# Kernel tuning notes

Measured on AMD Instinct MI355X. Metric: run time of the kernel, lower is better.

## Reference

```python
import jax, jax.numpy as jnp
import numpy as np

N = 100000   # nodes
E = 1600000  # edges
G = 1024     # graphs
V = 51       # attr_dims[0]+1 embedding rows (padding_idx=0)
EMB = 32
H = 2        # heads
D = 64       # hidden_dim (per-head out channels)
DC = H * D   # 128 = dim_conv
NEG_GAT = 0.2   # PyG GATConv default negative_slope
NEG_ACT = 0.05  # module's leaky_relu slope
LN_EPS = 1e-5


def setup_inputs() -> dict:
    key = jax.random.key(0)
    ks = jax.random.split(key, 20)
    def nrm(k, shape, scale=0.1):
        return jax.random.normal(k, shape, dtype=jnp.float32) * scale
    x = jax.random.randint(ks[0], (N, 1), 0, V)
    edge_index = jax.random.randint(ks[1], (2, E), 0, N)
    batch_idx = jnp.sort(jax.random.randint(ks[2], (N,), 0, G))
    return {
        'x': x, 'edge_index': edge_index, 'batch_idx': batch_idx,
        'emb': nrm(ks[3], (V, EMB)).at[0].set(0.0),  # padding_idx=0
        'ln_g': jnp.ones((EMB,), jnp.float32), 'ln_b': jnp.zeros((EMB,), jnp.float32),
        'W1': nrm(ks[4], (EMB, DC)), 'a_src1': nrm(ks[5], (H, D)), 'a_dst1': nrm(ks[6], (H, D)), 'b1': nrm(ks[7], (DC,)),
        'W2': nrm(ks[8], (DC, DC)), 'a_src2': nrm(ks[9], (H, D)), 'a_dst2': nrm(ks[10], (H, D)), 'b2': nrm(ks[11], (DC,)),
        'gw1': nrm(ks[12], (DC, D)), 'gb1': nrm(ks[13], (D,)),
        'gw2': nrm(ks[14], (D, 1)), 'gb2': nrm(ks[15], (1,)),
    }


def _gat_conv(xf, src, dst, W, a_src, a_dst, b):
    # xf: [N, in]; returns [N, H*D]. PyG GATConv, eval mode (attn dropout off).
    xw = (xf @ W).reshape(N, H, D)                           # [N,H,D]
    al_s = jnp.einsum('nhd,hd->nh', xw, a_src)
    al_d = jnp.einsum('nhd,hd->nh', xw, a_dst)
    e = jax.nn.leaky_relu(al_s[src] + al_d[dst], NEG_GAT)    # [E',H]
    m = jax.ops.segment_max(e, dst, num_segments=N)
    ex = jnp.exp(e - m[dst])
    s = jax.ops.segment_sum(ex, dst, num_segments=N)
    alpha = ex / s[dst]                                      # segment softmax over incoming edges
    msg = xw[src] * alpha[:, :, None]                        # [E',H,D]
    out = jax.ops.segment_sum(msg, dst, num_segments=N)      # [N,H,D]
    return out.reshape(N, DC) + b


def reference(x, edge_index, batch_idx, emb, ln_g, ln_b,
              W1, a_src1, a_dst1, b1, W2, a_src2, a_dst2, b2,
              gw1, gb1, gw2, gb2):
    # embedding + LayerNorm (dropout off in eval)
    xe = emb[x[:, 0]]                                        # [N,32]
    mu = jnp.mean(xe, axis=-1, keepdims=True)
    var = jnp.var(xe, axis=-1, keepdims=True)
    xe = (xe - mu) * jax.lax.rsqrt(var + LN_EPS) * ln_g + ln_b
    # add self loops (GATConv add_self_loops=True)
    ar = jnp.arange(N, dtype=edge_index.dtype)
    src = jnp.concatenate([edge_index[0], ar])
    dst = jnp.concatenate([edge_index[1], ar])
    h = jax.nn.leaky_relu(_gat_conv(xe, src, dst, W1, a_src1, a_dst1, b1), NEG_ACT)
    h = _gat_conv(h, src, dst, W2, a_src2, a_dst2, b2)       # [N,128]
    # attentional aggregation over graphs
    gate = jax.nn.leaky_relu(h @ gw1 + gb1, NEG_ACT) @ gw2 + gb2   # [N,1]
    gm = jax.ops.segment_max(gate, batch_idx, num_segments=G)
    ge = jnp.exp(gate - gm[batch_idx])
    gs = jax.ops.segment_sum(ge, batch_idx, num_segments=G)
    w = ge / gs[batch_idx]
    z = jax.ops.segment_sum(w * h, batch_idx, num_segments=G)      # [G,128]
    return h, z
```

## Files before the change

kernel.cpp:

```cpp
#include <hip/hip_runtime.h>
#include <hip/hip_bf16.h>
#include <stdint.h>

typedef unsigned short u16;
typedef unsigned int   u32;
typedef __attribute__((ext_vector_type(8))) short bf16x8;
typedef __attribute__((ext_vector_type(4))) float f32x4;

#define NEG_GAT 0.2f
#define NEG_ACT 0.05f
#define LN_EPS  1e-5f
#define NPARAM  15

__device__ __forceinline__ float bf2f(u32 bits16){
  union { u32 u; float f; } v; v.u = bits16 << 16; return v.f;
}
__device__ __forceinline__ u16 f2bf(float f){
  union { float f; u32 u; } v; v.f = f;
  u32 u = v.u;
  u32 r = (u + 0x7fffu + ((u >> 16) & 1u)) >> 16;
  return (u16)r;
}
__device__ __forceinline__ float lrelu(float x, float s){ return fmaxf(x, s * x); }

__device__ __forceinline__ int geti(const int* __restrict__ p, int i, int enc){
  return p[enc ? (2 * i) : i];
}


struct CvtParams {
  const void* src[NPARAM];
  float*      dst[NPARAM];
  int         n[NPARAM];
};

__global__ void k_detect(const u32* __restrict__ ln_g_raw, const int* __restrict__ ei_raw,
                         int* __restrict__ fflag, int* __restrict__ iflag,
                         int* __restrict__ errflag)
{
  if (threadIdx.x == 0){
    *fflag = (ln_g_raw[0] == 0x3F800000u) ? 0 : 1;
    int zeros = 0;
    for (int j = 0; j < 64; j++) if (ei_raw[2 * j + 1] == 0) zeros++;
    *iflag = (zeros >= 60) ? 1 : 0;
    *errflag = 0;
  }
}

__global__ void k_convert(CvtParams P, const int* __restrict__ flag)
{
  const int pi  = blockIdx.y;
  const int idx = blockIdx.x * 256 + threadIdx.x;
  if (idx >= P.n[pi]) return;
  if (*flag == 0) P.dst[pi][idx] = ((const float*)P.src[pi])[idx];
  else            P.dst[pi][idx] = bf2f(((const u16*)P.src[pi])[idx]);
}


__global__ void k_check_sorted(const int* __restrict__ batch, const int* __restrict__ iflag,
                               int n, int* __restrict__ errflag)
{
  int i = blockIdx.x * 256 + threadIdx.x;
  if (i < n - 1){
    if (geti(batch, i, *iflag) > geti(batch, i + 1, *iflag)) atomicOr(errflag, 8);
  }
}

__global__ void k_check_x(const int* __restrict__ x, const int* __restrict__ iflag,
                          int n, int V, int* __restrict__ errflag)
{
  int i = blockIdx.x * 256 + threadIdx.x;
  if (i < n){
    int v = geti(x, i, *iflag);
    if ((unsigned)v >= (unsigned)V) atomicOr(errflag, 16);
  }
}

__global__ void k_check_edges(const int* __restrict__ ei, const int* __restrict__ iflag,
                              int E, int n, int* __restrict__ errflag)
{
  int e = blockIdx.x * 256 + threadIdx.x;
  if (e < E){
    int enc = *iflag;
    int s = geti(ei, e, enc);
    int d = geti(ei, E + e, enc);
    if ((unsigned)s >= (unsigned)n || (unsigned)d >= (unsigned)n) atomicOr(errflag, 32);
  }
}


__global__ void k_hist(const int* __restrict__ ei, const int* __restrict__ iflag,
                       int* __restrict__ counts, int E, int n)
{
  int e = blockIdx.x * 256 + threadIdx.x;
  if (e < E){
    int d = geti(ei, E + e, *iflag);
    d = min(max(d, 0), n - 1);
    atomicAdd(&counts[d], 1);
  }
}

__global__ void k_scanA(const int* __restrict__ counts, int* __restrict__ rowptr,
                        int* __restrict__ bsums, int n)
{
  __shared__ int sd[1024];
  int tid = threadIdx.x;
  int gid = blockIdx.x * 1024 + tid;
  int v = (gid < n) ? counts[gid] : 0;
  sd[tid] = v;
  __syncthreads();
  for (int off = 1; off < 1024; off <<= 1){
    int t = 0;
    if (tid >= off) t = sd[tid - off];
    __syncthreads();
    if (tid >= off) sd[tid] += t;
    __syncthreads();
  }
  if (gid < n) rowptr[gid] = sd[tid] - v;
  if (tid == 1023) bsums[blockIdx.x] = sd[1023];
}

__global__ void k_scanB(const int* __restrict__ bsums, int* __restrict__ boffs, int nb)
{
  __shared__ int sd[128];
  int tid = threadIdx.x;
  int v = (tid < nb) ? bsums[tid] : 0;
  sd[tid] = v;
  __syncthreads();
  for (int off = 1; off < 128; off <<= 1){
    int t = 0;
    if (tid >= off) t = sd[tid - off];
    __syncthreads();
    if (tid >= off) sd[tid] += t;
    __syncthreads();
  }
  if (tid < nb) boffs[tid] = sd[tid] - v;
}

__global__ void k_scanC(int* __restrict__ rowptr, const int* __restrict__ boffs,
                        int* __restrict__ cursor, int n, int Etot)
{
  int gid = blockIdx.x * 1024 + threadIdx.x;
  if (gid < n){
    int v = rowptr[gid] + boffs[blockIdx.x];
    rowptr[gid] = v;
    cursor[gid] = v;
  }
  if (gid == 0) rowptr[n] = Etot;
}

__global__ void k_scatter(const int* __restrict__ ei, const int* __restrict__ iflag,
                          int* __restrict__ cursor, int* __restrict__ csr, int E, int n)
{
  int e = blockIdx.x * 256 + threadIdx.x;
  if (e < E){
    int enc = *iflag;
    int s = geti(ei, e, enc);
    int d = geti(ei, E + e, enc);
    d = min(max(d, 0), n - 1);
    int pos = atomicAdd(&cursor[d], 1);
    csr[pos] = s;
  }
}

__global__ void k_check_rows(const int* __restrict__ rowptr, const int* __restrict__ cursor,
                             int n, int* __restrict__ errflag)
{
  int i = blockIdx.x * 256 + threadIdx.x;
  if (i < n){
    if (cursor[i] != rowptr[i + 1]) atomicOr(errflag, 1);
    if (i == 0 && rowptr[0] != 0)   atomicOr(errflag, 4);
  }
}

__global__ void k_check_csr(const int* __restrict__ csr, int E, int n, int* __restrict__ errflag)
{
  int e = blockIdx.x * 256 + threadIdx.x;
  if (e < E && (unsigned)csr[e] >= (unsigned)n) atomicOr(errflag, 2);
}


#define BSH   9
#define BSZ   512
#define BMSK  511
#define MAXB  2048
#define BINB  8192
#define BTH   512

__global__ void k_bhist(const int* __restrict__ ei, const int* __restrict__ iflag,
                        int* __restrict__ bcnt, int E, int N, int nbuck)
{
  __shared__ int h[MAXB];
  const int t = threadIdx.x;
  for (int i = t; i < nbuck; i += 256) h[i] = 0;
  __syncthreads();
  const int enc = *iflag;
  for (int e = blockIdx.x * 256 + t; e < E; e += gridDim.x * 256){
    int d = geti(ei, E + e, enc);
    d = min(max(d, 0), N - 1);
    atomicAdd(&h[d >> BSH], 1);
  }
  __syncthreads();
  for (int i = t; i < nbuck; i += 256){
    int c = h[i];
    if (c) atomicAdd(&bcnt[i], c);
  }
}

__global__ void k_bscan(const int* __restrict__ bcnt, int* __restrict__ boff,
                        int* __restrict__ gcur, int* __restrict__ rowptr,
                        int nbuck, int N, int E)
{
  __shared__ int sd[MAXB];
  const int lane = threadIdx.x;
  for (int i = lane; i < nbuck; i += 64) sd[i] = bcnt[i];
  __syncthreads();
  const int L = (nbuck + 63) >> 6;
  const int b0 = lane * L;
  int sum = 0;
  for (int j = 0; j < L; j++){ int idx = b0 + j; if (idx < nbuck) sum += sd[idx]; }
  int excl = sum;
  for (int off = 1; off < 64; off <<= 1){
    int x = __shfl_up(excl, off);
    if (lane >= off) excl += x;
  }
  excl -= sum;
  int run = excl;
  for (int j = 0; j < L; j++){
    int idx = b0 + j;
    if (idx < nbuck){ boff[idx] = run; gcur[idx] = run; run += sd[idx]; }
  }
  if (lane == 0){ boff[nbuck] = E; rowptr[N] = E; }
}

__global__ __launch_bounds__(BTH) void k_bbin(
    const int* __restrict__ ei, const int* __restrict__ iflag,
    int* __restrict__ gcur, u32* __restrict__ binned,
    int E, int N, int nbuck)
{
  __shared__ u32 stage[BINB];
  __shared__ u16 sbk[BINB];
  __shared__ int hist[MAXB];
  __shared__ int base[MAXB];
  __shared__ int gpos[MAXB];
  const int t   = threadIdx.x;
  const int e0  = blockIdx.x * BINB;
  const int cnt = min(BINB, E - e0);
  const int enc = *iflag;

  for (int i = t; i < nbuck; i += BTH) hist[i] = 0;
  __syncthreads();

  u32 pv[16]; int bk[16]; int rk[16];
  #pragma unroll
  for (int k = 0; k < 16; k++){
    bk[k] = -1;
    int lo = k * BTH + t;
    if (lo < cnt){
      int e = e0 + lo;
      int s = geti(ei, e, enc);
      int d = geti(ei, E + e, enc);
      s = min(max(s, 0), N - 1);
      d = min(max(d, 0), N - 1);
      int b = d >> BSH;
      pv[k] = ((u32)s << BSH) | (u32)(d & BMSK);
      bk[k] = b;
      rk[k] = atomicAdd(&hist[b], 1);
    }
  }
  __syncthreads();

  if (t < 64){
    const int L = (nbuck + 63) >> 6;
    const int b0 = t * L;
    int sum = 0;
    for (int j = 0; j < L; j++){ int idx = b0 + j; if (idx < nbuck) sum += hist[idx]; }
    int excl = sum;
    for (int off = 1; off < 64; off <<= 1){
      int x = __shfl_up(excl, off);
      if (t >= off) excl += x;
    }
    excl -= sum;
    int run = excl;
    for (int j = 0; j < L; j++){
      int idx = b0 + j;
      if (idx < nbuck){ base[idx] = run; run += hist[idx]; }
    }
  }
  __syncthreads();

  for (int i = t; i < nbuck; i += BTH){
    int c = hist[i];
    gpos[i] = c ? atomicAdd(&gcur[i], c) : 0;
  }
  __syncthreads();

  #pragma unroll
  for (int k = 0; k < 16; k++){
    if (bk[k] >= 0){
      int slot = base[bk[k]] + rk[k];
      stage[slot] = pv[k];
      sbk[slot]   = (u16)bk[k];
    }
  }
  __syncthreads();

  for (int j = t; j < cnt; j += BTH){
    int b = sbk[j];
    binned[gpos[b] + (j - base[b])] = stage[j];
  }
}

__global__ __launch_bounds__(256) void k_bcsr(
    const u32* __restrict__ binned, const int* __restrict__ boff,
    int* __restrict__ rowptr, int* __restrict__ csr, int N, int nbuck)
{
  __shared__ int cnt[BSZ];
  __shared__ int rp[BSZ];
  __shared__ int cur[BSZ];
  const int b = blockIdx.x;
  const int t = threadIdx.x;
  const int lo = boff[b], hi = boff[b + 1];

  for (int i = t; i < BSZ; i += 256){ cnt[i] = 0; cur[i] = 0; }
  __syncthreads();

  for (int j = lo + t; j < hi; j += 256)
    atomicAdd(&cnt[binned[j] & BMSK], 1);
  __syncthreads();

  if (t < 64){
    const int b0 = t * 8;
    int sum = 0;
    #pragma unroll
    for (int j = 0; j < 8; j++) sum += cnt[b0 + j];
    int excl = sum;
    for (int off = 1; off < 64; off <<= 1){
      int x = __shfl_up(excl, off);
      if (t >= off) excl += x;
    }
    excl -= sum;
    int run = excl;
    #pragma unroll
    for (int j = 0; j < 8; j++){ rp[b0 + j] = run; run += cnt[b0 + j]; }
  }
  __syncthreads();

  const int node0 = b << BSH;
  for (int i = t; i < BSZ; i += 256){
    int node = node0 + i;
    if (node < N) rowptr[node] = lo + rp[i];
  }

  for (int j = lo + t; j < hi; j += 256){
    u32 pvv = binned[j];
    int dl  = pvv & BMSK;
    int pos = lo + rp[dl] + atomicAdd(&cur[dl], 1);
    csr[pos] = (int)(pvv >> BSH);
  }
}


__global__ void k_stamp_if(const int* __restrict__ errflag, float* __restrict__ out, int nel)
{
  int f = *errflag;
  if (f == 0) return;
  float s = 500.0f + 100.0f * (float)f;
  int i = blockIdx.x * 256 + threadIdx.x;
  if (i < nel) out[i] = s;
}

__global__ void k_stamp(float* __restrict__ out, int nel, float val)
{
  int i = blockIdx.x * 256 + threadIdx.x;
  if (i < nel) out[i] = val;
}


__global__ void k_prep(const float* __restrict__ emb,
                       const float* __restrict__ ln_g, const float* __restrict__ ln_b,
                       const float* __restrict__ W1, const float* __restrict__ a_src,
                       const float* __restrict__ a_dst,
                       u16* __restrict__ xwv, float* __restrict__ alsv, float* __restrict__ aldv)
{
  __shared__ float se[32];
  __shared__ float stats[2];
  __shared__ float sxw[128];
  const int v = blockIdx.x, t = threadIdx.x;
  if (t < 32) se[t] = emb[v * 32 + t];
  __syncthreads();
  if (t == 0){
    float s1 = 0.f, s2 = 0.f;
    for (int k = 0; k < 32; k++){ s1 += se[k]; s2 += se[k] * se[k]; }
    float mu = s1 * (1.f / 32.f);
    float var = s2 * (1.f / 32.f) - mu * mu;
    stats[0] = mu; stats[1] = rsqrtf(var + LN_EPS);
  }
  __syncthreads();
  const float mu = stats[0], rs = stats[1];
  float o = 0.f;
  for (int k = 0; k < 32; k++){
    float xe = (se[k] - mu) * rs * ln_g[k] + ln_b[k];
    o += xe * W1[k * 128 + t];
  }
  sxw[t] = o;
  xwv[v * 128 + t] = f2bf(o);
  __syncthreads();
  if (t < 2){
    float ps = 0.f, pd = 0.f;
    for (int d = 0; d < 64; d++){
      float vv = sxw[t * 64 + d];
      ps += vv * a_src[t * 64 + d];
      pd += vv * a_dst[t * 64 + d];
    }
    alsv[2 * v + t] = ps;
    aldv[2 * v + t] = pd;
  }
}


__global__ __launch_bounds__(256, 4) void k_gatw1(
    const int* __restrict__ rowptr, const int* __restrict__ csr,
    const int* __restrict__ x, const int* __restrict__ iflag,
    const float* __restrict__ alsv, const float* __restrict__ aldv,
    const u16* __restrict__ xwv, const float* __restrict__ bias,
    int N, int V, float* __restrict__ out)
{
  extern __shared__ char smem[];
  u16*    sxwv  = (u16*)smem;
  float2* sals  = (float2*)(smem + (size_t)V * 256);
  float2* sald  = sals + V;
  float4* sedge = (float4*)(smem + (size_t)V * 256 + (size_t)V * 16);

  const int tid = threadIdx.x;
  const int enc = *iflag;

  {
    const uint4* gx = (const uint4*)xwv;
    uint4* lx = (uint4*)sxwv;
    for (int idx = tid; idx < V * 16; idx += 256) lx[idx] = gx[idx];
    const float2* ga = (const float2*)alsv;
    const float2* gd = (const float2*)aldv;
    for (int idx = tid; idx < V; idx += 256){ sals[idx] = ga[idx]; sald[idx] = gd[idx]; }
  }
  __syncthreads();

  const int wave = tid >> 6;
  const int lane = tid & 63;
  const int sub  = lane >> 4;
  const int c16  = lane & 15;
  float4* mst = sedge + wave * 64;

  for (int i = blockIdx.x * 4 + wave; i < N; i += gridDim.x * 4){
    const int r0 = rowptr[i], deg = rowptr[i + 1] - r0, total = deg + 1;
    int vi = geti(x, i, enc); vi = min(max(vi, 0), V - 1);
    const float2 ad = sald[vi];

    float sum0 = 0.f, sum1 = 0.f;
    float acc[8];
    #pragma unroll
    for (int r = 0; r < 8; r++) acc[r] = 0.f;

    if (total <= 64){
      int vs = vi;
      float a0 = -3.0e38f, a1 = -3.0e38f;
      if (lane < total){
        int s = (lane < deg) ? csr[r0 + lane] : i;
        int v = geti(x, s, enc);
        vs = min(max(v, 0), V - 1);
        float2 as = sals[vs];
        a0 = lrelu(as.x + ad.x, NEG_GAT);
// ... 96 lines not shown
    int V, float* __restrict__ out)
{
  const int i    = blockIdx.x;
  const int lane = threadIdx.x;
  const int sub  = lane >> 4;
  const int c16  = lane & 15;
  const int enc  = *iflag;
  const int r0 = rowptr[i], deg = rowptr[i + 1] - r0, total = deg + 1;
  int vi = geti(x, i, enc); vi = min(max(vi, 0), V - 1);
  const float ad0 = aldv[2 * vi], ad1 = aldv[2 * vi + 1];

  float sum0 = 0.f, sum1 = 0.f;
  float acc[8];
  #pragma unroll
  for (int r = 0; r < 8; r++) acc[r] = 0.f;

  float m0 = -3.0e38f, m1 = -3.0e38f;
  for (int k = lane; k < total; k += 64){
    int s = (k < deg) ? csr[r0 + k] : i;
    int v = geti(x, s, enc); v = min(max(v, 0), V - 1);
    float2 as = *(const float2*)(alsv + 2 * v);
    m0 = fmaxf(m0, lrelu(as.x + ad0, NEG_GAT));
    m1 = fmaxf(m1, lrelu(as.y + ad1, NEG_GAT));
  }
  #pragma unroll
  for (int off = 32; off; off >>= 1){
    m0 = fmaxf(m0, __shfl_xor(m0, off));
    m1 = fmaxf(m1, __shfl_xor(m1, off));
  }
  for (int base = 0; base < total; base += 64){
    int k = base + lane;
    int vs = vi; float ex0 = 0.f, ex1 = 0.f;
    if (k < total){
      int s = (k < deg) ? csr[r0 + k] : i;
      int v = geti(x, s, enc); vs = min(max(v, 0), V - 1);
      float2 as = *(const float2*)(alsv + 2 * vs);
      ex0 = __expf(lrelu(as.x + ad0, NEG_GAT) - m0);
      ex1 = __expf(lrelu(as.y + ad1, NEG_GAT) - m1);
    }
    sum0 += ex0; sum1 += ex1;
    int cnt = min(64, total - base);
    int qmax = (cnt + 3) & ~3;
    for (int q = 0; q < qmax; q += 4){
      int   j  = q + sub;
      int   vj = __shfl(vs, j);
      float e0 = __shfl(ex0, j);
      float e1 = __shfl(ex1, j);
      float ej = (c16 < 8) ? e0 : e1;
      uint4 w = *(const uint4*)(xwv + (size_t)vj * 128 + c16 * 8);
      acc[0] += ej * bf2f(w.x & 0xffffu); acc[1] += ej * bf2f(w.x >> 16);
      acc[2] += ej * bf2f(w.y & 0xffffu); acc[3] += ej * bf2f(w.y >> 16);
      acc[4] += ej * bf2f(w.z & 0xffffu); acc[5] += ej * bf2f(w.z >> 16);
      acc[6] += ej * bf2f(w.w & 0xffffu); acc[7] += ej * bf2f(w.w >> 16);
    }
  }

  #pragma unroll
  for (int off = 32; off; off >>= 1){
    sum0 += __shfl_xor(sum0, off);
    sum1 += __shfl_xor(sum1, off);
  }
  #pragma unroll
  for (int r = 0; r < 8; r++){
    acc[r] += __shfl_xor(acc[r], 16);
    acc[r] += __shfl_xor(acc[r], 32);
  }

  if (sub == 0){
    float inv = 1.f / ((c16 < 8) ? sum0 : sum1);
    const float4* bp = (const float4*)(bias + c16 * 8);
    float4 b0 = bp[0], b1 = bp[1];
    float4 o0, o1;
    o0.x = lrelu(acc[0] * inv + b0.x, NEG_ACT); o0.y = lrelu(acc[1] * inv + b0.y, NEG_ACT);
    o0.z = lrelu(acc[2] * inv + b0.z, NEG_ACT); o0.w = lrelu(acc[3] * inv + b0.w, NEG_ACT);
    o1.x = lrelu(acc[4] * inv + b1.x, NEG_ACT); o1.y = lrelu(acc[5] * inv + b1.y, NEG_ACT);
    o1.z = lrelu(acc[6] * inv + b1.z, NEG_ACT); o1.w = lrelu(acc[7] * inv + b1.w, NEG_ACT);
    float* op = out + (size_t)i * 128 + c16 * 8;
    *(float4*)op       = o0;
    *(float4*)(op + 4) = o1;
  }
}


__global__ __launch_bounds__(256, 4) void k_gatw2(
    const int* __restrict__ rowptr, const int* __restrict__ csr,
    const float* __restrict__ al_s, const float* __restrict__ al_d,
    const u16* __restrict__ xw, const float* __restrict__ bias,
    int apply_act, int N, float* __restrict__ out)
{
  __shared__ float4 sedge[4][64];
  const int tid  = threadIdx.x;
  const int wave = tid >> 6;
  const int lane = tid & 63;
  const int sub  = lane >> 4;
  const int c16  = lane & 15;
  float4* mst = sedge[wave];

  for (int i = blockIdx.x * 4 + wave; i < N; i += gridDim.x * 4){
    const int r0 = rowptr[i], deg = rowptr[i + 1] - r0, total = deg + 1;
    const float2 ad = *(const float2*)(al_d + 2 * i);

    float sum0 = 0.f, sum1 = 0.f;
    float acc[8];
    #pragma unroll
    for (int r = 0; r < 8; r++) acc[r] = 0.f;

    if (total <= 64){
      int s = i;
      float a0 = -3.0e38f, a1 = -3.0e38f;
      if (lane < total){
        s = (lane < deg) ? csr[r0 + lane] : i;
        float2 as = *(const float2*)(al_s + 2 * s);
        a0 = lrelu(as.x + ad.x, NEG_GAT);
        a1 = lrelu(as.y + ad.y, NEG_GAT);
      }
      float m0 = a0, m1 = a1;
      #pragma unroll
      for (int off = 32; off; off >>= 1){
        m0 = fmaxf(m0, __shfl_xor(m0, off));
        m1 = fmaxf(m1, __shfl_xor(m1, off));
      }
      float ex0 = 0.f, ex1 = 0.f;
      if (lane < total){ ex0 = __expf(a0 - m0); ex1 = __expf(a1 - m1); }
      sum0 = ex0; sum1 = ex1;
      mst[lane] = make_float4(__int_as_float(s), ex0, ex1, 0.f);
      int qmax = (total + 3) & ~3;
      float4 md = mst[sub];
      uint4  w  = *(const uint4*)(xw + (size_t)__float_as_int(md.x) * 128 + c16 * 8);
      for (int q = 0; q < qmax; q += 4){
        float ej = (c16 < 8) ? md.y : md.z;
        uint4 wc = w;
        if (q + 4 < qmax){
          md = mst[q + 4 + sub];
          w  = *(const uint4*)(xw + (size_t)__float_as_int(md.x) * 128 + c16 * 8);
        }
        acc[0] += ej * bf2f(wc.x & 0xffffu); acc[1] += ej * bf2f(wc.x >> 16);
        acc[2] += ej * bf2f(wc.y & 0xffffu); acc[3] += ej * bf2f(wc.y >> 16);
        acc[4] += ej * bf2f(wc.z & 0xffffu); acc[5] += ej * bf2f(wc.z >> 16);
        acc[6] += ej * bf2f(wc.w & 0xffffu); acc[7] += ej * bf2f(wc.w >> 16);
      }
    } else {
      float m0 = -3.0e38f, m1 = -3.0e38f;
      for (int k = lane; k < total; k += 64){
        int s = (k < deg) ? csr[r0 + k] : i;
        float2 as = *(const float2*)(al_s + 2 * s);
        m0 = fmaxf(m0, lrelu(as.x + ad.x, NEG_GAT));
        m1 = fmaxf(m1, lrelu(as.y + ad.y, NEG_GAT));
      }
      #pragma unroll
      for (int off = 32; off; off >>= 1){
        m0 = fmaxf(m0, __shfl_xor(m0, off));
        m1 = fmaxf(m1, __shfl_xor(m1, off));
      }
      for (int base = 0; base < total; base += 64){
        int k = base + lane;
        int s = i; float ex0 = 0.f, ex1 = 0.f;
        if (k < total){
          s = (k < deg) ? csr[r0 + k] : i;
          float2 as = *(const float2*)(al_s + 2 * s);
          ex0 = __expf(lrelu(as.x + ad.x, NEG_GAT) - m0);
          ex1 = __expf(lrelu(as.y + ad.y, NEG_GAT) - m1);
        }
        sum0 += ex0; sum1 += ex1;
        mst[lane] = make_float4(__int_as_float(s), ex0, ex1, 0.f);
        int cnt = min(64, total - base);
        int qmax = (cnt + 3) & ~3;
        for (int q = 0; q < qmax; q += 4){
          float4 md = mst[q + sub];
          float ej = (c16 < 8) ? md.y : md.z;
          uint4 w = *(const uint4*)(xw + (size_t)__float_as_int(md.x) * 128 + c16 * 8);
          acc[0] += ej * bf2f(w.x & 0xffffu); acc[1] += ej * bf2f(w.x >> 16);
          acc[2] += ej * bf2f(w.y & 0xffffu); acc[3] += ej * bf2f(w.y >> 16);
          acc[4] += ej * bf2f(w.z & 0xffffu); acc[5] += ej * bf2f(w.z >> 16);
          acc[6] += ej * bf2f(w.w & 0xffffu); acc[7] += ej * bf2f(w.w >> 16);
        }
      }
    }

    #pragma unroll
    for (int off = 32; off; off >>= 1){
      sum0 += __shfl_xor(sum0, off);
      sum1 += __shfl_xor(sum1, off);
    }
    #pragma unroll
    for (int r = 0; r < 8; r++){
      acc[r] += __shfl_xor(acc[r], 16);
      acc[r] += __shfl_xor(acc[r], 32);
    }

    if (sub == 0){
      float inv = 1.f / ((c16 < 8) ? sum0 : sum1);
      const float4* bp = (const float4*)(bias + c16 * 8);
      float4 b0 = bp[0], b1 = bp[1];
      float4 o0, o1;
      o0.x = acc[0] * inv + b0.x; o0.y = acc[1] * inv + b0.y;
      o0.z = acc[2] * inv + b0.z; o0.w = acc[3] * inv + b0.w;
      o1.x = acc[4] * inv + b1.x; o1.y = acc[5] * inv + b1.y;
      o1.z = acc[6] * inv + b1.z; o1.w = acc[7] * inv + b1.w;
      if (apply_act){
        o0.x = lrelu(o0.x, NEG_ACT); o0.y = lrelu(o0.y, NEG_ACT);
        o0.z = lrelu(o0.z, NEG_ACT); o0.w = lrelu(o0.w, NEG_ACT);
        o1.x = lrelu(o1.x, NEG_ACT); o1.y = lrelu(o1.y, NEG_ACT);
        o1.z = lrelu(o1.z, NEG_ACT); o1.w = lrelu(o1.w, NEG_ACT);
      }
      float* op = out + (size_t)i * 128 + c16 * 8;
      *(float4*)op       = o0;
      *(float4*)(op + 4) = o1;
    }
  }
}


__global__ void k_packW(const float* __restrict__ W, int ncols, int ntiles,
                        u16* __restrict__ pb)
{
  const int ktile = blockIdx.x / ntiles;
  const int ntile = blockIdx.x % ntiles;
  const int lane  = threadIdx.x;
  const int n  = ntile * 16 + (lane & 15);
  const int k0 = ktile * 32 + (lane >> 4) * 8;
  u16* dst = pb + ((size_t)blockIdx.x * 64 + lane) * 8;
  #pragma unroll
  for (int j = 0; j < 8; j++)
    dst[j] = f2bf(W[(k0 + j) * ncols + n]);
}


__global__ __launch_bounds__(256, 2) void k_node2m(
    const float* __restrict__ h1, const u16* __restrict__ pb2,
    const float* __restrict__ a_src, const float* __restrict__ a_dst,
    int N, u16* __restrict__ xw, float* __restrict__ al_s, float* __restrict__ al_d)
{
  const int wave = threadIdx.x >> 6;
  const int lane = threadIdx.x & 63;
  const int rowbase = blockIdx.x * 64 + wave * 16;
  const int m    = lane & 15;
  const int quad = lane >> 4;

  int arow = rowbase + m; if (arow >= N) arow = N - 1;
  const float* aptr = h1 + (size_t)arow * 128 + quad * 8;

  f32x4 acc[8];
  #pragma unroll
  for (int nt = 0; nt < 8; nt++) acc[nt] = (f32x4){0.f, 0.f, 0.f, 0.f};

  #pragma unroll
  for (int kt = 0; kt < 4; kt++){
    float4 a0 = *(const float4*)(aptr + kt * 32);
    float4 a1 = *(const float4*)(aptr + kt * 32 + 4);
    bf16x8 af;
    af[0] = (short)f2bf(a0.x); af[1] = (short)f2bf(a0.y);
    af[2] = (short)f2bf(a0.z); af[3] = (short)f2bf(a0.w);
    af[4] = (short)f2bf(a1.x); af[5] = (short)f2bf(a1.y);
    af[6] = (short)f2bf(a1.z); af[7] = (short)f2bf(a1.w);
    const u16* bbase = pb2 + (((size_t)kt * 8) * 64 + lane) * 8;
    #pragma unroll
    for (int nt = 0; nt < 8; nt++){
      bf16x8 bf = *(const bf16x8*)(bbase + (size_t)nt * 64 * 8);
      acc[nt] = __builtin_amdgcn_mfma_f32_16x16x32_bf16(af, bf, acc[nt], 0, 0, 0);
    }
  }

  float asv[8], adv[8];
  #pragma unroll
  for (int nt = 0; nt < 8; nt++){
    asv[nt] = a_src[nt * 16 + m];
    adv[nt] = a_dst[nt * 16 + m];
  }
  #pragma unroll
  for (int r = 0; r < 4; r++){
    int row = rowbase + quad * 4 + r;
    bool ok = row < N;
    float s0 = 0.f, s1 = 0.f, d0 = 0.f, d1 = 0.f;
    #pragma unroll
    for (int nt = 0; nt < 8; nt++){
      float v = acc[nt][r];
      if (ok) xw[(size_t)row * 128 + nt * 16 + m] = f2bf(v);
      if (nt < 4){ s0 += v * asv[nt]; d0 += v * adv[nt]; }
      else       { s1 += v * asv[nt]; d1 += v * adv[nt]; }
    }
    #pragma unroll
    for (int off = 1; off < 16; off <<= 1){
      s0 += __shfl_xor(s0, off); s1 += __shfl_xor(s1, off);
      d0 += __shfl_xor(d0, off); d1 += __shfl_xor(d1, off);
    }
    if (ok && m == 0){
      al_s[2 * row] = s0; al_s[2 * row + 1] = s1;
      al_d[2 * row] = d0; al_d[2 * row + 1] = d1;
    }
  }
}


__global__ __launch_bounds__(256, 2) void k_gatem(
    const float* __restrict__ h, const u16* __restrict__ pbg,
    const float* __restrict__ gb1, const float* __restrict__ gw2,
    const float* __restrict__ gb2, int N, float* __restrict__ gate)
{
  const int wave = threadIdx.x >> 6;
  const int lane = threadIdx.x & 63;
  const int rowbase = blockIdx.x * 64 + wave * 16;
  const int m    = lane & 15;
  const int quad = lane >> 4;

  int arow = rowbase + m; if (arow >= N) arow = N - 1;
  const float* aptr = h + (size_t)arow * 128 + quad * 8;

// ... 93 lines not shown
extern "C" void kernel_launch(void* const* d_in, const int* in_sizes, int n_in,
                              void* d_out, int out_size, void* d_ws, size_t ws_size,
                              hipStream_t stream)
{
  const int* x      = (const int*)d_in[0];
  const int* ei     = (const int*)d_in[1];
  const int* batch  = (const int*)d_in[2];

  const int N = in_sizes[0];
  const int E = in_sizes[1] / 2;
  const int V = in_sizes[3] / 32;
  const int G = out_size / 128 - N;

  char* p = (char*)d_ws;
  auto alloc = [&](size_t bytes) -> char* {
    char* r = p; p += (bytes + 255) & ~(size_t)255; return r;
  };
  int*   multi  = (int*)  alloc((size_t)N * 4);
  int*   rowptr = (int*)  alloc((size_t)(N + 1) * 4);
  int*   csr    = (int*)  alloc((size_t)E * 4);
  int*   bsums  = (int*)  alloc(4096);
  int*   boffs  = (int*)  alloc(4096);
  int*   flags  = (int*)  alloc(256);
  int*   fflag  = flags;
  int*   iflag  = flags + 1;
  int*   errflg = flags + 2;
  float* al_s   = (float*)alloc((size_t)N * 2 * 4);
  float* al_d   = (float*)alloc((size_t)N * 2 * 4);
  u16*   xw     = (u16*)  alloc((size_t)N * 128 * 2);
  u16*   xwv    = (u16*)  alloc((size_t)V * 128 * 2);
  float* alsv   = (float*)alloc((size_t)V * 2 * 4);
  float* aldv   = (float*)alloc((size_t)V * 2 * 4);
  u16*   pb2    = (u16*)  alloc((size_t)128 * 128 * 2);
  u16*   pbg    = (u16*)  alloc((size_t)128 * 64 * 2);

  const int nbuck = (N + BSZ - 1) >> BSH;
  int*   bcnt   = (int*)  alloc((size_t)(MAXB) * 4);
  int*   boff   = (int*)  alloc((size_t)(MAXB + 1) * 4);
  int*   gcur   = (int*)  alloc((size_t)(MAXB) * 4);
  u32*   binned = (u32*)  alloc((size_t)E * 4);

  CvtParams cp;
  float* fpar[NPARAM];
  int maxn = 0;
  for (int pi = 0; pi < NPARAM; pi++){
    int n = in_sizes[3 + pi];
    fpar[pi] = (float*)alloc((size_t)n * 4);
    cp.src[pi] = d_in[3 + pi];
    cp.dst[pi] = fpar[pi];
    cp.n[pi]   = n;
    if (n > maxn) maxn = n;
  }
  const size_t needed = (size_t)(p - (char*)d_ws);

  const float* emb    = fpar[0];
  const float* ln_g   = fpar[1];
  const float* ln_b   = fpar[2];
  const float* W1     = fpar[3];
  const float* a_src1 = fpar[4];
  const float* a_dst1 = fpar[5];
  const float* b1     = fpar[6];
  const float* W2     = fpar[7];
  const float* a_src2 = fpar[8];
  const float* a_dst2 = fpar[9];
  const float* b2     = fpar[10];
  const float* gw1    = fpar[11];
  const float* gb1    = fpar[12];
  const float* gw2    = fpar[13];
  const float* gb2    = fpar[14];
  (void)n_in;

  int ob = (out_size + 255) / 256;
  if (ws_size < needed){
    k_stamp<<<ob, 256, 0, stream>>>((float*)d_out, out_size, 9999.0f);
    return;
  }

  int*   counts = multi;
  int*   cursor = multi;
  float* gate   = (float*)multi;
  float* hbuf   = (float*)d_out;
  float* zbuf   = (float*)d_out + (size_t)N * 128;

  k_detect<<<1, 64, 0, stream>>>((const u32*)d_in[4], ei, fflag, iflag, errflg);
  dim3 cgrid((maxn + 255) / 256, NPARAM);
  k_convert<<<cgrid, 256, 0, stream>>>(cp, fflag);

  int eb = (E + 255) / 256;
  int nb = (N + 1023) / 1024;
  int nb256 = (N + 255) / 256;

  k_check_sorted<<<nb256, 256, 0, stream>>>(batch, iflag, N, errflg);
  k_check_x<<<nb256, 256, 0, stream>>>(x, iflag, N, V, errflg);
  k_check_edges<<<eb, 256, 0, stream>>>(ei, iflag, E, N, errflg);

  if (nbuck <= MAXB){
    hipMemsetAsync(bcnt, 0, (size_t)nbuck * 4, stream);
    k_bhist<<<256, 256, 0, stream>>>(ei, iflag, bcnt, E, N, nbuck);
    k_bscan<<<1, 64, 0, stream>>>(bcnt, boff, gcur, rowptr, nbuck, N, E);
    k_bbin<<<(E + BINB - 1) / BINB, BTH, 0, stream>>>(ei, iflag, gcur, binned, E, N, nbuck);
    k_bcsr<<<nbuck, 256, 0, stream>>>(binned, boff, rowptr, csr, N, nbuck);
  } else {
    hipMemsetAsync(counts, 0, (size_t)N * 4, stream);
    hipMemsetAsync(csr, 0xFF, (size_t)E * 4, stream);
    k_hist<<<eb, 256, 0, stream>>>(ei, iflag, counts, E, N);
    k_scanA<<<nb, 1024, 0, stream>>>(counts, rowptr, bsums, N);
    k_scanB<<<1, 128, 0, stream>>>(bsums, boffs, nb);
    k_scanC<<<nb, 1024, 0, stream>>>(rowptr, boffs, cursor, N, E);
    k_scatter<<<eb, 256, 0, stream>>>(ei, iflag, cursor, csr, E, N);
    k_check_rows<<<nb256, 256, 0, stream>>>(rowptr, cursor, N, errflg);
    k_check_csr<<<eb, 256, 0, stream>>>(csr, E, N, errflg);
  }

  k_packW<<<32, 64, 0, stream>>>(W2, 128, 8, pb2);
  k_packW<<<16, 64, 0, stream>>>(gw1, 64, 4, pbg);

  k_prep<<<V, 128, 0, stream>>>(emb, ln_g, ln_b, W1, a_src1, a_dst1, xwv, alsv, aldv);

  const int gwb = min(2048, (N + 3) / 4);
  const size_t smem1 = (size_t)V * 272 + 4096;
  if (smem1 <= 64 * 1024){
    k_gatw1<<<gwb, 256, smem1, stream>>>(rowptr, csr, x, iflag, alsv, aldv, xwv, b1, N, V, hbuf);
  } else {
    k_gatw1g<<<N, 64, 0, stream>>>(rowptr, csr, x, iflag, alsv, aldv, xwv, b1, V, hbuf);
  }

  const int gblk = (N + 63) / 64;
  k_node2m<<<gblk, 256, 0, stream>>>(hbuf, pb2, a_src2, a_dst2, N, xw, al_s, al_d);

  k_gatw2<<<gwb, 256, 0, stream>>>(rowptr, csr, al_s, al_d, xw, b2, 0, N, hbuf);

  k_gatem<<<gblk, 256, 0, stream>>>(hbuf, pbg, gb1, gw2, gb2, N, gate);
  k_graphsw<<<G, 256, 0, stream>>>(batch, iflag, gate, hbuf, zbuf, N);

  k_stamp_if<<<ob, 256, 0, stream>>>(errflg, (float*)d_out, out_size);
}
```

Baseline: 381.5 us.

## Merge validation and table-prep launches, fold edge check into binning, one-wave-per-node GAT2

```diff
diff --git a/kernel.cpp b/kernel.cpp
--- a/kernel.cpp
+++ b/kernel.cpp
@@ -34,16 +34,20 @@
   int         n[NPARAM];
 };
 
+#define MAXB  2048
+
 __global__ void k_detect(const u32* __restrict__ ln_g_raw, const int* __restrict__ ei_raw,
-                         int* __restrict__ fflag, int* __restrict__ iflag,
-                         int* __restrict__ errflag)
-{
-  if (threadIdx.x == 0){
-    *fflag = (ln_g_raw[0] == 0x3F800000u) ? 0 : 1;
+                         int* __restrict__ flags, int* __restrict__ bcnt)
+{
+  const int t = threadIdx.x;
+  for (int i = t; i < MAXB; i += 256) bcnt[i] = 0;
+  if (t == 0){
+    flags[0] = (ln_g_raw[0] == 0x3F800000u) ? 0 : 1;
     int zeros = 0;
     for (int j = 0; j < 64; j++) if (ei_raw[2 * j + 1] == 0) zeros++;
-    *iflag = (zeros >= 60) ? 1 : 0;
-    *errflag = 0;
+    flags[1] = (zeros >= 60) ? 1 : 0;
+    flags[2] = 0;
+    flags[3] = 0;
   }
 }
 
@@ -57,22 +61,16 @@
 }
 
 
-__global__ void k_check_sorted(const int* __restrict__ batch, const int* __restrict__ iflag,
-                               int n, int* __restrict__ errflag)
+__global__ void k_checks(const int* __restrict__ batch, const int* __restrict__ x,
+                         const int* __restrict__ iflag,
+                         int n, int V, int* __restrict__ errflag)
 {
   int i = blockIdx.x * 256 + threadIdx.x;
-  if (i < n - 1){
-    if (geti(batch, i, *iflag) > geti(batch, i + 1, *iflag)) atomicOr(errflag, 8);
-  }
-}
-
-__global__ void k_check_x(const int* __restrict__ x, const int* __restrict__ iflag,
-                          int n, int V, int* __restrict__ errflag)
-{
-  int i = blockIdx.x * 256 + threadIdx.x;
+  const int enc = *iflag;
   if (i < n){
-    int v = geti(x, i, *iflag);
+    int v = geti(x, i, enc);
     if ((unsigned)v >= (unsigned)V) atomicOr(errflag, 16);
+    if (i < n - 1 && geti(batch, i, enc) > geti(batch, i + 1, enc)) atomicOr(errflag, 8);
   }
 }
 
@@ -183,7 +181,6 @@
 #define BSH   9
 #define BSZ   512
 #define BMSK  511
-#define MAXB  2048
 #define BINB  8192
 #define BTH   512
 
@@ -236,7 +233,7 @@
 __global__ __launch_bounds__(BTH) void k_bbin(
     const int* __restrict__ ei, const int* __restrict__ iflag,
     int* __restrict__ gcur, u32* __restrict__ binned,
-    int E, int N, int nbuck)
+    int E, int N, int nbuck, int* __restrict__ errflag)
 {
   __shared__ u32 stage[BINB];
   __shared__ u16 sbk[BINB];
@@ -252,6 +249,7 @@
   __syncthreads();
 
   u32 pv[16]; int bk[16]; int rk[16];
+  int bad = 0;
   #pragma unroll
   for (int k = 0; k < 16; k++){
     bk[k] = -1;
@@ -260,6 +258,7 @@
       int e = e0 + lo;
       int s = geti(ei, e, enc);
       int d = geti(ei, E + e, enc);
+      if ((unsigned)s >= (unsigned)N || (unsigned)d >= (unsigned)N) bad = 1;
       s = min(max(s, 0), N - 1);
       d = min(max(d, 0), N - 1);
       int b = d >> BSH;
@@ -268,6 +267,7 @@
       rk[k] = atomicAdd(&hist[b], 1);
     }
   }
+  if (bad) atomicOr(errflag, 32);
   __syncthreads();
 
   if (t < 64){
@@ -377,16 +377,40 @@
 }
 
 
-__global__ void k_prep(const float* __restrict__ emb,
-                       const float* __restrict__ ln_g, const float* __restrict__ ln_b,
-                       const float* __restrict__ W1, const float* __restrict__ a_src,
-                       const float* __restrict__ a_dst,
-                       u16* __restrict__ xwv, float* __restrict__ alsv, float* __restrict__ aldv)
-{
+__global__ __launch_bounds__(128) void k_tables(
+    const float* __restrict__ emb,
+    const float* __restrict__ ln_g, const float* __restrict__ ln_b,
+    const float* __restrict__ W1, const float* __restrict__ a_src,
+    const float* __restrict__ a_dst,
+    const float* __restrict__ W2, const float* __restrict__ gw1,
+    int V,
+    u16* __restrict__ xwv, float* __restrict__ alsv, float* __restrict__ aldv,
+    u16* __restrict__ pb2, u16* __restrict__ pbg)
+{
+  const int bid = blockIdx.x;
+  const int t   = threadIdx.x;
+
+  if (bid >= V){
+    if (t >= 64) return;
+    int pw = bid - V;
+    const float* W; int ncols, ntiles, blk; u16* pb;
+    if (pw < 32){ W = W2; ncols = 128; ntiles = 8; blk = pw;      pb = pb2; }
+    else        { W = gw1; ncols = 64;  ntiles = 4; blk = pw - 32; pb = pbg; }
+    const int ktile = blk / ntiles;
+    const int ntile = blk % ntiles;
+    const int n  = ntile * 16 + (t & 15);
+    const int k0 = ktile * 32 + (t >> 4) * 8;
+    u16* dst = pb + ((size_t)blk * 64 + t) * 8;
+    #pragma unroll
+    for (int j = 0; j < 8; j++)
+      dst[j] = f2bf(W[(k0 + j) * ncols + n]);
+    return;
+  }
+
   __shared__ float se[32];
   __shared__ float stats[2];
   __shared__ float sxw[128];
-  const int v = blockIdx.x, t = threadIdx.x;
+  const int v = bid;
   if (t < 32) se[t] = emb[v * 32 + t];
   __syncthreads();
   if (t == 0){
@@ -649,147 +673,125 @@
 }
 
 
-__global__ __launch_bounds__(256, 4) void k_gatw2(
+__global__ __launch_bounds__(64, 8) void k_gatw2(
     const int* __restrict__ rowptr, const int* __restrict__ csr,
     const float* __restrict__ al_s, const float* __restrict__ al_d,
     const u16* __restrict__ xw, const float* __restrict__ bias,
-    int apply_act, int N, float* __restrict__ out)
-{
-  __shared__ float4 sedge[4][64];
-  const int tid  = threadIdx.x;
-  const int wave = tid >> 6;
-  const int lane = tid & 63;
+    int apply_act, float* __restrict__ out)
+{
+  const int i    = blockIdx.x;
+  const int lane = threadIdx.x;
   const int sub  = lane >> 4;
   const int c16  = lane & 15;
-  float4* mst = sedge[wave];
-
-  for (int i = blockIdx.x * 4 + wave; i < N; i += gridDim.x * 4){
-    const int r0 = rowptr[i], deg = rowptr[i + 1] - r0, total = deg + 1;
-    const float2 ad = *(const float2*)(al_d + 2 * i);
-
-    float sum0 = 0.f, sum1 = 0.f;
-    float acc[8];
-    #pragma unroll
-    for (int r = 0; r < 8; r++) acc[r] = 0.f;
-
-    if (total <= 64){
-      int s = i;
-      float a0 = -3.0e38f, a1 = -3.0e38f;
-      if (lane < total){
-        s = (lane < deg) ? csr[r0 + lane] : i;
+  const int r0 = rowptr[i], deg = rowptr[i + 1] - r0, total = deg + 1;
+  const float2 ad = *(const float2*)(al_d + 2 * i);
+
+  float sum0 = 0.f, sum1 = 0.f;
+  float acc[8];
+  #pragma unroll
+  for (int r = 0; r < 8; r++) acc[r] = 0.f;
+
+  if (total <= 64){
+    int s = i;
+    float a0 = -3.0e38f, a1 = -3.0e38f;
+    if (lane < total){
+      s = (lane < deg) ? csr[r0 + lane] : i;
+      float2 as = *(const float2*)(al_s + 2 * s);
+      a0 = lrelu(as.x + ad.x, NEG_GAT);
+      a1 = lrelu(as.y + ad.y, NEG_GAT);
+    }
+    float m0 = a0, m1 = a1;
+    #pragma unroll
+    for (int off = 32; off; off >>= 1){
+      m0 = fmaxf(m0, __shfl_xor(m0, off));
+      m1 = fmaxf(m1, __shfl_xor(m1, off));
+    }
+    float ex0 = 0.f, ex1 = 0.f;
+    if (lane < total){ ex0 = __expf(a0 - m0); ex1 = __expf(a1 - m1); }
+    sum0 = ex0; sum1 = ex1;
+    int qmax = (total + 3) & ~3;
+    for (int q = 0; q < qmax; q += 4){
+      int   j  = q + sub;
+      int   sj = __shfl(s, j);
+      float e0 = __shfl(ex0, j);
+      float e1 = __shfl(ex1, j);
+      float ej = (c16 < 8) ? e0 : e1;
+      uint4 w = *(const uint4*)(xw + (size_t)sj * 128 + c16 * 8);
+      acc[0] += ej * bf2f(w.x & 0xffffu); acc[1] += ej * bf2f(w.x >> 16);
+      acc[2] += ej * bf2f(w.y & 0xffffu); acc[3] += ej * bf2f(w.y >> 16);
+      acc[4] += ej * bf2f(w.z & 0xffffu); acc[5] += ej * bf2f(w.z >> 16);
+      acc[6] += ej * bf2f(w.w & 0xffffu); acc[7] += ej * bf2f(w.w >> 16);
+    }
+  } else {
+    float m0 = -3.0e38f, m1 = -3.0e38f;
+    for (int k = lane; k < total; k += 64){
+      int s = (k < deg) ? csr[r0 + k] : i;
+      float2 as = *(const float2*)(al_s + 2 * s);
+      m0 = fmaxf(m0, lrelu(as.x + ad.x, NEG_GAT));
+      m1 = fmaxf(m1, lrelu(as.y + ad.y, NEG_GAT));
+    }
+    #pragma unroll
+    for (int off = 32; off; off >>= 1){
+      m0 = fmaxf(m0, __shfl_xor(m0, off));
+      m1 = fmaxf(m1, __shfl_xor(m1, off));
+    }
+    for (int base = 0; base < total; base += 64){
+      int k = base + lane;
+      int s = i; float ex0 = 0.f, ex1 = 0.f;
+      if (k < total){
+        s = (k < deg) ? csr[r0 + k] : i;
         float2 as = *(const float2*)(al_s + 2 * s);
-        a0 = lrelu(as.x + ad.x, NEG_GAT);
-        a1 = lrelu(as.y + ad.y, NEG_GAT);
+        ex0 = __expf(lrelu(as.x + ad.x, NEG_GAT) - m0);
+        ex1 = __expf(lrelu(as.y + ad.y, NEG_GAT) - m1);
       }
-      float m0 = a0, m1 = a1;
-      #pragma unroll
-      for (int off = 32; off; off >>= 1){
-        m0 = fmaxf(m0, __shfl_xor(m0, off));
-        m1 = fmaxf(m1, __shfl_xor(m1, off));
+      sum0 += ex0; sum1 += ex1;
+      int cnt = min(64, total - base);
+      int qmax = (cnt + 3) & ~3;
+      for (int q = 0; q < qmax; q += 4){
+        int   j  = q + sub;
+        int   sj = __shfl(s, j);
+        float e0 = __shfl(ex0, j);
+        float e1 = __shfl(ex1, j);
+        float ej = (c16 < 8) ? e0 : e1;
+        uint4 w = *(const uint4*)(xw + (size_t)sj * 128 + c16 * 8);
+        acc[0] += ej * bf2f(w.x & 0xffffu); acc[1] += ej * bf2f(w.x >> 16);
+        acc[2] += ej * bf2f(w.y & 0xffffu); acc[3] += ej * bf2f(w.y >> 16);
+        acc[4] += ej * bf2f(w.z & 0xffffu); acc[5] += ej * bf2f(w.z >> 16);
+        acc[6] += ej * bf2f(w.w & 0xffffu); acc[7] += ej * bf2f(w.w >> 16);
       }
-      float ex0 = 0.f, ex1 = 0.f;
-      if (lane < total){ ex0 = __expf(a0 - m0); ex1 = __expf(a1 - m1); }
-      sum0 = ex0; sum1 = ex1;
-      mst[lane] = make_float4(__int_as_float(s), ex0, ex1, 0.f);
-      int qmax = (total + 3) & ~3;
-      float4 md = mst[sub];
-      uint4  w  = *(const uint4*)(xw + (size_t)__float_as_int(md.x) * 128 + c16 * 8);
-      for (int q = 0; q < qmax; q += 4){
-        float ej = (c16 < 8) ? md.y : md.z;
-        uint4 wc = w;
-        if (q + 4 < qmax){
-          md = mst[q + 4 + sub];
-          w  = *(const uint4*)(xw + (size_t)__float_as_int(md.x) * 128 + c16 * 8);
-        }
-        acc[0] += ej * bf2f(wc.x & 0xffffu); acc[1] += ej * bf2f(wc.x >> 16);
-        acc[2] += ej * bf2f(wc.y & 0xffffu); acc[3] += ej * bf2f(wc.y >> 16);
-        acc[4] += ej * bf2f(wc.z & 0xffffu); acc[5] += ej * bf2f(wc.z >> 16);
-        acc[6] += ej * bf2f(wc.w & 0xffffu); acc[7] += ej * bf2f(wc.w >> 16);
-      }
-    } else {
-      float m0 = -3.0e38f, m1 = -3.0e38f;
-      for (int k = lane; k < total; k += 64){
-        int s = (k < deg) ? csr[r0 + k] : i;
-        float2 as = *(const float2*)(al_s + 2 * s);
-        m0 = fmaxf(m0, lrelu(as.x + ad.x, NEG_GAT));
-        m1 = fmaxf(m1, lrelu(as.y + ad.y, NEG_GAT));
-      }
-      #pragma unroll
-      for (int off = 32; off; off >>= 1){
-        m0 = fmaxf(m0, __shfl_xor(m0, off));
-        m1 = fmaxf(m1, __shfl_xor(m1, off));
-      }
-      for (int base = 0; base < total; base += 64){
-        int k = base + lane;
-        int s = i; float ex0 = 0.f, ex1 = 0.f;
-        if (k < total){
-          s = (k < deg) ? csr[r0 + k] : i;
-          float2 as = *(const float2*)(al_s + 2 * s);
-          ex0 = __expf(lrelu(as.x + ad.x, NEG_GAT) - m0);
-          ex1 = __expf(lrelu(as.y + ad.y, NEG_GAT) - m1);
-        }
-        sum0 += ex0; sum1 += ex1;
-        mst[lane] = make_float4(__int_as_float(s), ex0, ex1, 0.f);
-        int cnt = min(64, total - base);
-        int qmax = (cnt + 3) & ~3;
-        for (int q = 0; q < qmax; q += 4){
-          float4 md = mst[q + sub];
-          float ej = (c16 < 8) ? md.y : md.z;
-          uint4 w = *(const uint4*)(xw + (size_t)__float_as_int(md.x) * 128 + c16 * 8);
-          acc[0] += ej * bf2f(w.x & 0xffffu); acc[1] += ej * bf2f(w.x >> 16);
-          acc[2] += ej * bf2f(w.y & 0xffffu); acc[3] += ej * bf2f(w.y >> 16);
-          acc[4] += ej * bf2f(w.z & 0xffffu); acc[5] += ej * bf2f(w.z >> 16);
-          acc[6] += ej * bf2f(w.w & 0xffffu); acc[7] += ej * bf2f(w.w >> 16);
-        }
-      }
-    }
-
-    #pragma unroll
-    for (int off = 32; off; off >>= 1){
-      sum0 += __shfl_xor(sum0, off);
-      sum1 += __shfl_xor(sum1, off);
-    }
-    #pragma unroll
-    for (int r = 0; r < 8; r++){
-      acc[r] += __shfl_xor(acc[r], 16);
-      acc[r] += __shfl_xor(acc[r], 32);
-    }
-
-    if (sub == 0){
-      float inv = 1.f / ((c16 < 8) ? sum0 : sum1);
-      const float4* bp = (const float4*)(bias + c16 * 8);
-      float4 b0 = bp[0], b1 = bp[1];
-      float4 o0, o1;
-      o0.x = acc[0] * inv + b0.x; o0.y = acc[1] * inv + b0.y;
-      o0.z = acc[2] * inv + b0.z; o0.w = acc[3] * inv + b0.w;
-      o1.x = acc[4] * inv + b1.x; o1.y = acc[5] * inv + b1.y;
-      o1.z = acc[6] * inv + b1.z; o1.w = acc[7] * inv + b1.w;
-      if (apply_act){
-        o0.x = lrelu(o0.x, NEG_ACT); o0.y = lrelu(o0.y, NEG_ACT);
-        o0.z = lrelu(o0.z, NEG_ACT); o0.w = lrelu(o0.w, NEG_ACT);
-        o1.x = lrelu(o1.x, NEG_ACT); o1.y = lrelu(o1.y, NEG_ACT);
-        o1.z = lrelu(o1.z, NEG_ACT); o1.w = lrelu(o1.w, NEG_ACT);
-      }
-      float* op = out + (size_t)i * 128 + c16 * 8;
-      *(float4*)op       = o0;
-      *(float4*)(op + 4) = o1;
-    }
-  }
-}
-
-
-__global__ void k_packW(const float* __restrict__ W, int ncols, int ntiles,
-                        u16* __restrict__ pb)
-{
-  const int ktile = blockIdx.x / ntiles;
-  const int ntile = blockIdx.x % ntiles;
-  const int lane  = threadIdx.x;
-  const int n  = ntile * 16 + (lane & 15);
-  const int k0 = ktile * 32 + (lane >> 4) * 8;
-  u16* dst = pb + ((size_t)blockIdx.x * 64 + lane) * 8;
-  #pragma unroll
-  for (int j = 0; j < 8; j++)
-    dst[j] = f2bf(W[(k0 + j) * ncols + n]);
+    }
+  }
+
+  #pragma unroll
+  for (int off = 32; off; off >>= 1){
+    sum0 += __shfl_xor(sum0, off);
+    sum1 += __shfl_xor(sum1, off);
+  }
+  #pragma unroll
+  for (int r = 0; r < 8; r++){
+    acc[r] += __shfl_xor(acc[r], 16);
+    acc[r] += __shfl_xor(acc[r], 32);
+  }
+
+  if (sub == 0){
+    float inv = 1.f / ((c16 < 8) ? sum0 : sum1);
+    const float4* bp = (const float4*)(bias + c16 * 8);
+    float4 b0 = bp[0], b1 = bp[1];
+    float4 o0, o1;
+    o0.x = acc[0] * inv + b0.x; o0.y = acc[1] * inv + b0.y;
+    o0.z = acc[2] * inv + b0.z; o0.w = acc[3] * inv + b0.w;
+    o1.x = acc[4] * inv + b1.x; o1.y = acc[5] * inv + b1.y;
+    o1.z = acc[6] * inv + b1.z; o1.w = acc[7] * inv + b1.w;
+    if (apply_act){
+      o0.x = lrelu(o0.x, NEG_ACT); o0.y = lrelu(o0.y, NEG_ACT);
+      o0.z = lrelu(o0.z, NEG_ACT); o0.w = lrelu(o0.w, NEG_ACT);
+      o1.x = lrelu(o1.x, NEG_ACT); o1.y = lrelu(o1.y, NEG_ACT);
+      o1.z = lrelu(o1.z, NEG_ACT); o1.w = lrelu(o1.w, NEG_ACT);
+    }
+    float* op = out + (size_t)i * 128 + c16 * 8;
+    *(float4*)op       = o0;
+    *(float4*)(op + 4) = o1;
+  }
 }
 
 
@@ -1049,7 +1051,7 @@
   float* hbuf   = (float*)d_out;
   float* zbuf   = (float*)d_out + (size_t)N * 128;
 
-  k_detect<<<1, 64, 0, stream>>>((const u32*)d_in[4], ei, fflag, iflag, errflg);
+  k_detect<<<1, 256, 0, stream>>>((const u32*)d_in[4], ei, flags, bcnt);
   dim3 cgrid((maxn + 255) / 256, NPARAM);
   k_convert<<<cgrid, 256, 0, stream>>>(cp, fflag);
 
@@ -1057,17 +1059,15 @@
   int nb = (N + 1023) / 1024;
   int nb256 = (N + 255) / 256;
 
-  k_check_sorted<<<nb256, 256, 0, stream>>>(batch, iflag, N, errflg);
-  k_check_x<<<nb256, 256, 0, stream>>>(x, iflag, N, V, errflg);
-  k_check_edges<<<eb, 256, 0, stream>>>(ei, iflag, E, N, errflg);
+  k_checks<<<nb256, 256, 0, stream>>>(batch, x, iflag, N, V, errflg);
 
   if (nbuck <= MAXB){
-    hipMemsetAsync(bcnt, 0, (size_t)nbuck * 4, stream);
     k_bhist<<<256, 256, 0, stream>>>(ei, iflag, bcnt, E, N, nbuck);
     k_bscan<<<1, 64, 0, stream>>>(bcnt, boff, gcur, rowptr, nbuck, N, E);
-    k_bbin<<<(E + BINB - 1) / BINB, BTH, 0, stream>>>(ei, iflag, gcur, binned, E, N, nbuck);
+    k_bbin<<<(E + BINB - 1) / BINB, BTH, 0, stream>>>(ei, iflag, gcur, binned, E, N, nbuck, errflg);
     k_bcsr<<<nbuck, 256, 0, stream>>>(binned, boff, rowptr, csr, N, nbuck);
   } else {
+    k_check_edges<<<eb, 256, 0, stream>>>(ei, iflag, E, N, errflg);
     hipMemsetAsync(counts, 0, (size_t)N * 4, stream);
     hipMemsetAsync(csr, 0xFF, (size_t)E * 4, stream);
     k_hist<<<eb, 256, 0, stream>>>(ei, iflag, counts, E, N);
@@ -1079,10 +1079,8 @@
     k_check_csr<<<eb, 256, 0, stream>>>(csr, E, N, errflg);
   }
 
-  k_packW<<<32, 64, 0, stream>>>(W2, 128, 8, pb2);
-  k_packW<<<16, 64, 0, stream>>>(gw1, 64, 4, pbg);
-
-  k_prep<<<V, 128, 0, stream>>>(emb, ln_g, ln_b, W1, a_src1, a_dst1, xwv, alsv, aldv);
+  k_tables<<<V + 48, 128, 0, stream>>>(emb, ln_g, ln_b, W1, a_src1, a_dst1,
+                                       W2, gw1, V, xwv, alsv, aldv, pb2, pbg);
 
   const int gwb = min(2048, (N + 3) / 4);
   const size_t smem1 = (size_t)V * 272 + 4096;
@@ -1095,7 +1093,7 @@
   const int gblk = (N + 63) / 64;
   k_node2m<<<gblk, 256, 0, stream>>>(hbuf, pb2, a_src2, a_dst2, N, xw, al_s, al_d);
 
-  k_gatw2<<<gwb, 256, 0, stream>>>(rowptr, csr, al_s, al_d, xw, b2, 0, N, hbuf);
+  k_gatw2<<<N, 64, 0, stream>>>(rowptr, csr, al_s, al_d, xw, b2, 0, hbuf);
 
   k_gatem<<<gblk, 256, 0, stream>>>(hbuf, pbg, gb1, gw2, gb2, N, gate);
   k_graphsw<<<G, 256, 0, stream>>>(batch, iflag, gate, hbuf, zbuf, N);
```

Result: no change. 375.7 us (-1.5%).
